# Optimization experiments

Hardware: AMD Instinct MI355X
Metric: run time of the kernel (lower is better)

## Reference

```python
import jax, jax.numpy as jnp
import numpy as np
from jax import lax


def _lstm_cell(x, h, c, W_ih, W_hh, b_ih, b_hh):
    # torch nn.LSTMCell: gates = x W_ih^T + b_ih + h W_hh^T + b_hh, order i,f,g,o
    gates = x @ W_ih.T + h @ W_hh.T + (b_ih + b_hh)
    i, f, g, o = jnp.split(gates, 4, axis=-1)
    c_new = jax.nn.sigmoid(f) * c + jax.nn.sigmoid(i) * jnp.tanh(g)
    h_new = jax.nn.sigmoid(o) * jnp.tanh(c_new)
    return h_new, c_new


def setup_inputs():
    key = jax.random.key(0)
    ks = jax.random.split(key, 10)
    B, S, E, H, V = 128, 20, 512, 512, 10000
    images = jax.random.normal(ks[0], (B, E), jnp.float32)
    captions = jax.random.randint(ks[1], (B, S), 0, V)
    length = jax.random.randint(ks[2], (B, 1), 2, S + 1)
    length = length.at[0, 0].set(S)  # guarantee max decode length == S-1 (static shape)
    s = 0.05
    emb = jax.random.normal(ks[3], (V, E), jnp.float32) * s
    W_ih = jax.random.normal(ks[4], (4 * H, E), jnp.float32) * s
    W_hh = jax.random.normal(ks[5], (4 * H, H), jnp.float32) * s
    b_ih = jax.random.normal(ks[6], (4 * H,), jnp.float32) * s
    b_hh = jax.random.normal(ks[7], (4 * H,), jnp.float32) * s
    fc_w = jax.random.normal(ks[8], (V, H), jnp.float32) * s
    fc_b = jax.random.normal(ks[9], (V,), jnp.float32) * s
    return dict(images=images, captions=captions, length=length, emb=emb,
                W_ih=W_ih, W_hh=W_hh, b_ih=b_ih, b_hh=b_hh, fc_w=fc_w, fc_b=fc_b)


def reference(images, captions, length, emb, W_ih, W_hh, b_ih, b_hh, fc_w, fc_b):
    B, S = captions.shape
    T = S - 1  # static max(decode_lengths) by construction
    H = W_hh.shape[1]
    lens = length[:, 0]
    sort_ind = jnp.argsort(-lens)  # stable descending sort, like torch .sort(descending=True)
    sorted_lens = lens[sort_ind]
    dec_len = sorted_lens - 1
    features = images[sort_ind]
    captions_s = captions[sort_ind]
    embeddings = emb[captions_s]  # [B, S, E]

    zeros = jnp.zeros((B, H), images.dtype)
    h, c = _lstm_cell(features, zeros, zeros, W_ih, W_hh, b_ih, b_hh)

    xs = (jnp.swapaxes(embeddings[:, :T, :], 0, 1), jnp.arange(T))  # [T,B,E], [T]

    def step(carry, x):
        h, c = carry
        x_t, t = x
        # ragged batch in the original == masking here: rows with dec_len<=t never
        # contribute to any future valid output (lengths sorted descending).
        h, c = _lstm_cell(x_t, h, c, W_ih, W_hh, b_ih, b_hh)
        preds = h @ fc_w.T + fc_b  # dropout is identity in eval mode
        preds = jnp.where((dec_len > t)[:, None], preds, 0.0)
        return (h, c), preds

    (_, _), preds = lax.scan(step, (h, c), xs)
    predictions = jnp.swapaxes(preds, 0, 1)  # [B, T, V]
    return predictions, captions_s, dec_len, sort_ind
```

## Files before the change

kernel.cpp:

```cpp
#include <hip/hip_runtime.h>

typedef float  f32x4 __attribute__((ext_vector_type(4)));
typedef short  s16x8 __attribute__((ext_vector_type(8)));
typedef unsigned short u16x4 __attribute__((ext_vector_type(4)));

#define MFMA16(a,b,c) __builtin_amdgcn_mfma_f32_16x16x32_bf16(a,b,c,0,0,0)

#define PRED_ELEMS 24320000ull

__device__ __forceinline__ unsigned short f2bf(float f){
  unsigned u = __builtin_bit_cast(unsigned, f);
  u += 0x7fffu + ((u >> 16) & 1u);
  return (unsigned short)(u >> 16);
}
__device__ __forceinline__ float sigf(float x){ return 1.0f/(1.0f + __expf(-x)); }
__device__ __forceinline__ float tanh_(float x){
  x = fminf(15.0f, fmaxf(-15.0f, x));
  float e = __expf(2.0f*x);
  return (e - 1.0f) / (e + 1.0f);
}
__device__ __forceinline__ s16x8 ld8(const unsigned short* p){
  return *reinterpret_cast<const s16x8*>(p);
}
__device__ __forceinline__ void gload_lds16(const unsigned short* src, unsigned short* dst){
  __builtin_amdgcn_global_load_lds(
      (const __attribute__((address_space(1))) void*)src,
      (__attribute__((address_space(3))) void*)dst, 16, 0, 0);
}

__global__ void k0_sort(const int* __restrict__ length, const int* __restrict__ captions,
                        float* __restrict__ out, int* __restrict__ sortp,
                        int* __restrict__ nactp, unsigned int* __restrict__ cnt4k)
{
  __shared__ int sl[128], sdl[128], ssi[128];
  int tid = threadIdx.x;
  for (int k = tid; k < 1024; k += 128) cnt4k[k] = 0u;
  if (tid < 128) sl[tid] = length[tid];
  __syncthreads();
  if (tid < 128){
    int l = sl[tid];
    int rank = 0;
    for (int j = 0; j < 128; ++j){
      int lj = sl[j];
      rank += (lj > l) || (lj == l && j < tid);
    }
    sortp[rank] = tid;
    ssi[rank] = tid;   sdl[rank] = l - 1;
  }
  __syncthreads();
  if (tid < 20){
    int c = 0;
    for (int r = 0; r < 128; ++r) c += (sdl[r] >= tid);
    nactp[tid] = c;
  }
  if (tid < 128){
    const size_t P = PRED_ELEMS;
    int si = ssi[tid];
    for (int t = 0; t < 20; ++t) out[P + tid*20 + t] = (float)captions[si*20 + t];
    out[P + 2560 + tid] = (float)sdl[tid];
    out[P + 2688 + tid] = (float)si;
  }
}

__device__ __forceinline__ void cvt4(unsigned short* dst, const float* src, int u){
  f32x4 v = *reinterpret_cast<const f32x4*>(src + (size_t)u*4);
  u16x4 o;
  o[0]=f2bf(v[0]); o[1]=f2bf(v[1]); o[2]=f2bf(v[2]); o[3]=f2bf(v[3]);
  *reinterpret_cast<u16x4*>(dst + (size_t)u*4) = o;
}

__global__ void k1_convert(const float* __restrict__ images, const int* __restrict__ captions,
    const float* __restrict__ emb, const float* __restrict__ wih, const float* __restrict__ whh,
    const float* __restrict__ bih, const float* __restrict__ bhh, const float* __restrict__ fcw,
    const int* __restrict__ sortp,
    unsigned short* __restrict__ wihb, unsigned short* __restrict__ whhb,
    unsigned short* __restrict__ fcwb, float* __restrict__ biasp,
    unsigned short* __restrict__ xseq, unsigned short* __restrict__ hseq,
    unsigned short* __restrict__ hloc)
{
  const int U0 = 262144;
  const int U1 = 262144;
  const int U2 = 1294336;
  const int U3 = 512;
  const int U4 = 327680;
  const int U5 = 16384;
  const int U6 = 16384;
  const int total = U0+U1+U2+U3+U4+U5+U6;
  for (int i = blockIdx.x*blockDim.x + threadIdx.x; i < total; i += gridDim.x*blockDim.x){
    int j = i;
    if (j < U0){ cvt4(wihb, wih, j); continue; }
    j -= U0;
    if (j < U1){ cvt4(whhb, whh, j); continue; }
    j -= U1;
    if (j < U2){
      int row = j >> 7;
      if (row < 10000) cvt4(fcwb, fcw, j);
      else { u16x4 z = {0,0,0,0}; *reinterpret_cast<u16x4*>(fcwb + (size_t)j*4) = z; }
      continue;
    }
    j -= U2;
    if (j < U3){
      int e0 = j*4;
      for (int e = 0; e < 4; ++e) biasp[e0+e] = bih[e0+e] + bhh[e0+e];
      continue;
    }
    j -= U3;
    if (j < U4){
      int elem = j*4;
      int s = elem >> 16;
      int rem = elem & 65535;
      int r = rem >> 9;
      int k = rem & 511;
      const float* src;
      if (s == 0) src = images + (size_t)sortp[r]*512 + k;
      else {
        int cap = captions[sortp[r]*20 + (s-1)];
        src = emb + (size_t)cap*512 + k;
      }
      f32x4 v = *reinterpret_cast<const f32x4*>(src);
      u16x4 o;
      o[0]=f2bf(v[0]); o[1]=f2bf(v[1]); o[2]=f2bf(v[2]); o[3]=f2bf(v[3]);
      *reinterpret_cast<u16x4*>(xseq + (size_t)j*4) = o;
      continue;
    }
    j -= U4;
    if (j < U5){ u16x4 z = {0,0,0,0}; *reinterpret_cast<u16x4*>(hseq + (size_t)j*4) = z; continue; }
    j -= U5;
    {
      int e0 = j*4;
      int x = e0 >> 13;
      int rem = e0 & 8191;
      u16x4 z = {0,0,0,0};
      *reinterpret_cast<u16x4*>(hloc + (size_t)x*172032 + rem) = z;
    }
  }
}

__global__ __launch_bounds__(256, 1) void lstm_chain(
    const unsigned short* __restrict__ xseq, const unsigned short* __restrict__ wih,
    const unsigned short* __restrict__ whh, const float* __restrict__ biasp,
    unsigned short* __restrict__ hseq, unsigned short* __restrict__ hloc,
    const int* __restrict__ nact, unsigned int* __restrict__ claimc,
    unsigned int* __restrict__ flags)
{
  const int tid = threadIdx.x;
  __shared__ int s_xw;
  __shared__ float pgh[4][4][16][17];
  __shared__ float pgx[4][4][16][17];
  __shared__ unsigned char lds_pad[51200];
  asm volatile("" : : "v"(&lds_pad[tid & 127]) : "memory");

  if (tid == 0){
    unsigned xcc;
    asm volatile("s_getreg_b32 %0, hwreg(20, 0, 4)" : "=s"(xcc));
    int x = (int)(xcc & 7u);
    unsigned slot = __hip_atomic_fetch_add(claimc + x*64, 1u,
                      __ATOMIC_RELAXED, __HIP_MEMORY_SCOPE_AGENT);
    s_xw = (x << 8) | (int)(slot & 255u);
  }
  __syncthreads();
  const int x = s_xw >> 8;
  const int w = s_xw & 255;
  if (w >= 32) return;
  const int R0 = x*16;
  const int C0 = w*16;
  unsigned int* myflags = flags + x*64;

  const int lane = tid & 63;
  const int kk   = tid >> 6;
  const int fr   = lane & 15;
  const int fkq  = (lane >> 4) * 8;
  const int rr   = (lane >> 4) * 4;

  s16x8 BI[4][4], BH[4][4];
  #pragma unroll
  for (int q = 0; q < 4; ++q)
    #pragma unroll
    for (int i = 0; i < 4; ++i){
      size_t off = (size_t)(q*512 + C0 + fr)*512 + kk*128 + i*32 + fkq;
      BI[q][i] = ld8(wih + off);
      BH[q][i] = ld8(whh + off);
    }

  unsigned short* hl = hloc + (size_t)x*172032;
  const int prow = tid >> 4;
  const int pcol = tid & 15;
  const float bz0 = biasp[       C0 + pcol];
  const float bz1 = biasp[ 512 + C0 + pcol];
  const float bz2 = biasp[1024 + C0 + pcol];
  const float bz3 = biasp[1536 + C0 + pcol];
  float creg = 0.f;

  {
    s16x8 ax[4];
    #pragma unroll
    for (int i = 0; i < 4; ++i)
      ax[i] = ld8(xseq + (R0 + fr)*512 + kk*128 + i*32 + fkq);
    #pragma unroll
    for (int q = 0; q < 4; ++q){
      f32x4 accx = (f32x4){0.f,0.f,0.f,0.f};
      #pragma unroll
      for (int i = 0; i < 4; ++i)
        accx = MFMA16(ax[i], BI[q][i], accx);
      #pragma unroll
      for (int p = 0; p < 4; ++p)
        pgx[kk][q][rr + p][fr] = accx[p];
    }
  }
  __syncthreads();

  for (int s = 0; s < 20; ++s){
    if (R0 >= nact[s]) break;
    const unsigned short* hp = hl + (size_t)s*8192;

    s16x8 ah[4];
    #pragma unroll
    for (int i = 0; i < 4; ++i)
      ah[i] = ld8(hp + fr*512 + kk*128 + i*32 + fkq);
    #pragma unroll
    for (int q = 0; q < 4; ++q){
      f32x4 acch = (f32x4){0.f,0.f,0.f,0.f};
      #pragma unroll
      for (int i = 0; i < 4; ++i)
        acch = MFMA16(ah[i], BH[q][i], acch);
      #pragma unroll
      for (int p = 0; p < 4; ++p)
        pgh[kk][q][rr + p][fr] = acch[p];
    }
    __syncthreads();

    unsigned short hb;
    {
      float iv = pgh[0][0][prow][pcol] + pgh[1][0][prow][pcol]
               + pgh[2][0][prow][pcol] + pgh[3][0][prow][pcol]
               + pgx[0][0][prow][pcol] + pgx[1][0][prow][pcol]
               + pgx[2][0][prow][pcol] + pgx[3][0][prow][pcol] + bz0;
      float fv = pgh[0][1][prow][pcol] + pgh[1][1][prow][pcol]
               + pgh[2][1][prow][pcol] + pgh[3][1][prow][pcol]
               + pgx[0][1][prow][pcol] + pgx[1][1][prow][pcol]
               + pgx[2][1][prow][pcol] + pgx[3][1][prow][pcol] + bz1;
      float gv = pgh[0][2][prow][pcol] + pgh[1][2][prow][pcol]
               + pgh[2][2][prow][pcol] + pgh[3][2][prow][pcol]
               + pgx[0][2][prow][pcol] + pgx[1][2][prow][pcol]
               + pgx[2][2][prow][pcol] + pgx[3][2][prow][pcol] + bz2;
      float ov = pgh[0][3][prow][pcol] + pgh[1][3][prow][pcol]
               + pgh[2][3][prow][pcol] + pgh[3][3][prow][pcol]
               + pgx[0][3][prow][pcol] + pgx[1][3][prow][pcol]
               + pgx[2][3][prow][pcol] + pgx[3][3][prow][pcol] + bz3;
      creg = sigf(fv)*creg + sigf(iv)*tanh_(gv);
      float h = sigf(ov)*tanh_(creg);
      hb = f2bf(h);
      hl[(size_t)(s+1)*8192 + prow*512 + C0 + pcol] = hb;
    }
    __syncthreads();

    hseq[(size_t)(s+1)*65536 + (R0 + prow)*512 + C0 + pcol] = hb;

    if (s < 19 && nact[s+1] > R0){
      const unsigned tgt = (unsigned)(s + 1);
      if (tid == 0)
        __hip_atomic_store(&myflags[w], tgt, __ATOMIC_RELAXED, __HIP_MEMORY_SCOPE_AGENT);

      {
        const unsigned short* xp = xseq + (size_t)(s+1)*65536;
        s16x8 ax[4];
        #pragma unroll
        for (int i = 0; i < 4; ++i)
          ax[i] = ld8(xp + (R0 + fr)*512 + kk*128 + i*32 + fkq);
        #pragma unroll
        for (int q = 0; q < 4; ++q){
          f32x4 accx = (f32x4){0.f,0.f,0.f,0.f};
          #pragma unroll
          for (int i = 0; i < 4; ++i)
            accx = MFMA16(ax[i], BI[q][i], accx);
          #pragma unroll
          for (int p = 0; p < 4; ++p)
            pgx[kk][q][rr + p][fr] = accx[p];
        }
      }

      if (tid < 64){
        long guard = 0;
        for (;;){
          bool ok = true;
          if (tid < 32)
            ok = (__hip_atomic_load(&myflags[tid], __ATOMIC_RELAXED,
                                    __HIP_MEMORY_SCOPE_AGENT) >= tgt);
          if (__all(ok) || ++guard > (1L << 20)) break;
          __builtin_amdgcn_s_sleep(1);
        }
      }
      __syncthreads();
    }
  }
}

__global__ __launch_bounds__(256) void fc_kernel(
    const unsigned short* __restrict__ hseq, const unsigned short* __restrict__ fcwb,
    const float* __restrict__ fcb, const int* __restrict__ nact,
    float* __restrict__ out)
{
  const int b    = blockIdx.x;
  const int x    = b & 7;
  const int slot = b >> 3;
  const int t    = slot % 19;
  const int p    = x + 8*(slot/19);
  if (p >= 79) return;
  const int v0   = p * 128;
  const int tid  = threadIdx.x;

  __shared__ unsigned short Ab[2][128*64];
  __shared__ unsigned short Bb[2][128*64];

  const unsigned short* Ag = hseq + (size_t)(t + 2)*65536;
  const unsigned short* Bg = fcwb + (size_t)v0*512;
  const int n_t = nact[t + 1];

  const int srow = tid >> 3;
  const int sphy = tid & 7;
  const int wuni = (tid >> 6) << 9;

  #define STAGE(gsrc, lbuf, kt)                                              \
    _Pragma("unroll")                                                        \
    for (int call = 0; call < 4; ++call){                                    \
      int row_ = call*32 + srow;                                             \
      gload_lds16(gsrc + (size_t)row_*512 + (kt)*64 + ((sphy ^ (row_ & 7)) << 3), \
                  lbuf + call*2048 + wuni);                                  \
    }

  const int lane = tid & 63;
  const int wv   = tid >> 6;
  const int wr   = wv >> 1, wc = wv & 1;
  const int fr   = lane & 15;
  const int hi   = lane >> 4;

  f32x4 acc[4][4];
  #pragma unroll
  for (int i = 0; i < 4; ++i)
    #pragma unroll
    for (int j = 0; j < 4; ++j)
      acc[i][j] = (f32x4){0.f,0.f,0.f,0.f};

  STAGE(Ag, Ab[0], 0)
  STAGE(Bg, Bb[0], 0)
  asm volatile("s_waitcnt vmcnt(0)" ::: "memory");
  __syncthreads();

  int cur = 0;
  for (int kt = 0; kt < 8; ++kt){
    if (kt < 7){
      STAGE(Ag, Ab[cur^1], kt+1)
      STAGE(Bg, Bb[cur^1], kt+1)
    }
    const unsigned short* As = Ab[cur];
    const unsigned short* Bs = Bb[cur];
    #pragma unroll
    for (int kk = 0; kk < 2; ++kk){
      const int c = kk*4 + hi;
      s16x8 af[4], bf[4];
      #pragma unroll
      for (int i = 0; i < 4; ++i){
        int row = wr*64 + i*16 + fr;
        af[i] = ld8(As + row*64 + ((c ^ (row & 7)) << 3));
      }
      #pragma unroll
      for (int j = 0; j < 4; ++j){
        int col = wc*64 + j*16 + fr;
        bf[j] = ld8(Bs + col*64 + ((c ^ (col & 7)) << 3));
      }
      #pragma unroll
      for (int i = 0; i < 4; ++i)
        #pragma unroll
        for (int j = 0; j < 4; ++j)
          acc[i][j] = MFMA16(af[i], bf[j], acc[i][j]);
    }
    asm volatile("s_waitcnt vmcnt(0)" ::: "memory");
    __syncthreads();
    cur ^= 1;
  }

  const int rr = hi * 4;
  #pragma unroll
  for (int j = 0; j < 4; ++j){
    int v = v0 + wc*64 + j*16 + fr;
    if (v >= 10000) continue;
    float bb = fcb[v];
    #pragma unroll
    for (int i = 0; i < 4; ++i){
      #pragma unroll
      for (int pp = 0; pp < 4; ++pp){
        int r = wr*64 + i*16 + rr + pp;
        out[(size_t)(r*19 + t)*10000 + v] = (r < n_t) ? (acc[i][j][pp] + bb) : 0.0f;
      }
    }
  }
  #undef STAGE
}

extern "C" void kernel_launch(void* const* d_in, const int* in_sizes, int n_in,
                              void* d_out, int out_size, void* d_ws, size_t ws_size,
                              hipStream_t stream) {
  const float* images   = (const float*)d_in[0];
  const int*   captions = (const int*)  d_in[1];
  const int*   length   = (const int*)  d_in[2];
  const float* emb      = (const float*)d_in[3];
  const float* W_ih     = (const float*)d_in[4];
  const float* W_hh     = (const float*)d_in[5];
  const float* b_ih     = (const float*)d_in[6];
  const float* b_hh     = (const float*)d_in[7];
  const float* fc_w     = (const float*)d_in[8];
  const float* fc_b     = (const float*)d_in[9];
  float* out = (float*)d_out;
  char*  ws  = (char*)d_ws;

  int*            sortp  = (int*)           (ws + 0);
  int*            nactp  = (int*)           (ws + 2048);
  float*          biasp  = (float*)         (ws + 4096);
  unsigned int*   cnt4k  = (unsigned int*)  (ws + 12288);
  unsigned int*   claimc = cnt4k;
  unsigned int*   flags  = cnt4k + 512;
  unsigned short* hloc   = (unsigned short*)(ws + 16384);
  unsigned short* hseq   = (unsigned short*)(ws + 2768896);
  unsigned short* xseq   = (unsigned short*)(ws + 5521408);
  unsigned short* wihb   = (unsigned short*)(ws + 8142848);
  unsigned short* whhb   = (unsigned short*)(ws + 10240000);
  unsigned short* fcwb   = (unsigned short*)(ws + 12337152);

  k0_sort<<<1, 128, 0, stream>>>(length, captions, out, sortp, nactp, cnt4k);
  k1_convert<<<4096, 256, 0, stream>>>(images, captions, emb, W_ih, W_hh, b_ih, b_hh,
                                       fc_w, sortp, wihb, whhb, fcwb, biasp, xseq, hseq, hloc);
  lstm_chain<<<256, 256, 0, stream>>>(xseq, wihb, whhb, biasp, hseq, hloc,
                                      nactp, claimc, flags);
  fc_kernel<<<1520, 256, 0, stream>>>(hseq, fcwb, fc_b, nactp, out);
}
```

Before: 122.9 us.

## Fuse LSTM recurrence and FC projection into one kernel with flag-based overlap

Merges the recurrent LSTM chain kernel and the vocabulary FC GEMM into a single launch. The first 256 blocks run the recurrence and publish a per-XCD step flag, while the remaining blocks wait on those flags and compute predictions for a timestep as soon as its hidden states are written. This lets the FC GEMM overlap the serial recurrence instead of waiting for it to finish. The FC tile is also re-staged with a smaller K chunk (32) and a different pipelining order so it fits the shared LDS union. The change depends on all chain blocks being co-resident with the waiting FC blocks, and the spin-waits could stall if scheduling does not guarantee that. Removing the LDS padding also changes occupancy for the chain blocks.

Result: slower. 148.0 us (+20.4%).

```diff
diff --git a/kernel.cpp b/kernel.cpp
--- a/kernel.cpp
+++ b/kernel.cpp
@@ -136,203 +136,234 @@
   }
 }
 
-__global__ __launch_bounds__(256, 1) void lstm_chain(
+union ShMem {
+  struct {
+    float pgh[4][4][16][17];
+    float pgx[4][4][16][17];
+    unsigned short mbuf[16][16];
+    int s_xw;
+  } l;
+  unsigned short arena[2][2][4096];
+};
+
+__global__ __launch_bounds__(256) void chain_fc(
     const unsigned short* __restrict__ xseq, const unsigned short* __restrict__ wih,
     const unsigned short* __restrict__ whh, const float* __restrict__ biasp,
     unsigned short* __restrict__ hseq, unsigned short* __restrict__ hloc,
+    const unsigned short* __restrict__ fcwb, const float* __restrict__ fcb,
     const int* __restrict__ nact, unsigned int* __restrict__ claimc,
-    unsigned int* __restrict__ flags)
+    unsigned int* __restrict__ flags, unsigned int* __restrict__ fcflag,
+    float* __restrict__ out)
 {
+  __shared__ ShMem sh;
   const int tid = threadIdx.x;
-  __shared__ int s_xw;
-  __shared__ float pgh[4][4][16][17];
-  __shared__ float pgx[4][4][16][17];
-  __shared__ unsigned char lds_pad[51200];
-  asm volatile("" : : "v"(&lds_pad[tid & 127]) : "memory");
-
-  if (tid == 0){
-    unsigned xcc;
-    asm volatile("s_getreg_b32 %0, hwreg(20, 0, 4)" : "=s"(xcc));
-    int x = (int)(xcc & 7u);
-    unsigned slot = __hip_atomic_fetch_add(claimc + x*64, 1u,
-                      __ATOMIC_RELAXED, __HIP_MEMORY_SCOPE_AGENT);
-    s_xw = (x << 8) | (int)(slot & 255u);
-  }
-  __syncthreads();
-  const int x = s_xw >> 8;
-  const int w = s_xw & 255;
-  if (w >= 32) return;
-  const int R0 = x*16;
-  const int C0 = w*16;
-  unsigned int* myflags = flags + x*64;
-
+  const int bid = blockIdx.x;
   const int lane = tid & 63;
-  const int kk   = tid >> 6;
-  const int fr   = lane & 15;
-  const int fkq  = (lane >> 4) * 8;
-  const int rr   = (lane >> 4) * 4;
-
-  s16x8 BI[4][4], BH[4][4];
-  #pragma unroll
-  for (int q = 0; q < 4; ++q)
-    #pragma unroll
-    for (int i = 0; i < 4; ++i){
-      size_t off = (size_t)(q*512 + C0 + fr)*512 + kk*128 + i*32 + fkq;
-      BI[q][i] = ld8(wih + off);
-      BH[q][i] = ld8(whh + off);
-    }
-
-  unsigned short* hl = hloc + (size_t)x*172032;
-  const int prow = tid >> 4;
-  const int pcol = tid & 15;
-  const float bz0 = biasp[       C0 + pcol];
-  const float bz1 = biasp[ 512 + C0 + pcol];
-  const float bz2 = biasp[1024 + C0 + pcol];
-  const float bz3 = biasp[1536 + C0 + pcol];
-  float creg = 0.f;
-
-  {
-    s16x8 ax[4];
-    #pragma unroll
-    for (int i = 0; i < 4; ++i)
-      ax[i] = ld8(xseq + (R0 + fr)*512 + kk*128 + i*32 + fkq);
-    #pragma unroll
-    for (int q = 0; q < 4; ++q){
-      f32x4 accx = (f32x4){0.f,0.f,0.f,0.f};
+
+  if (bid < 256){
+    if (tid == 0){
+      unsigned xcc;
+      asm volatile("s_getreg_b32 %0, hwreg(20, 0, 4)" : "=s"(xcc));
+      int x = (int)(xcc & 7u);
+      unsigned slot = __hip_atomic_fetch_add(claimc + x*64, 1u,
+                        __ATOMIC_RELAXED, __HIP_MEMORY_SCOPE_AGENT);
+      sh.l.s_xw = (x << 8) | (int)(slot & 255u);
+    }
+    __syncthreads();
+    const int x = sh.l.s_xw >> 8;
+    const int w = sh.l.s_xw & 255;
+    if (w >= 32) return;
+    const int R0 = x*16;
+    const int C0 = w*16;
+    unsigned int* myflags = flags + x*64;
+
+    const int kk  = tid >> 6;
+    const int fr  = lane & 15;
+    const int fkq = (lane >> 4) * 8;
+    const int rr  = (lane >> 4) * 4;
+
+    s16x8 BI[4][4], BH[4][4];
+    #pragma unroll
+    for (int q = 0; q < 4; ++q)
+      #pragma unroll
+      for (int i = 0; i < 4; ++i){
+        size_t off = (size_t)(q*512 + C0 + fr)*512 + kk*128 + i*32 + fkq;
+        BI[q][i] = ld8(wih + off);
+        BH[q][i] = ld8(whh + off);
+      }
+
+    unsigned short* hl = hloc + (size_t)x*172032;
+    const int prow = tid >> 4;
+    const int pcol = tid & 15;
+    const float bz0 = biasp[       C0 + pcol];
+    const float bz1 = biasp[ 512 + C0 + pcol];
+    const float bz2 = biasp[1024 + C0 + pcol];
+    const float bz3 = biasp[1536 + C0 + pcol];
+    float creg = 0.f;
+
+    {
+      s16x8 ax[4];
       #pragma unroll
       for (int i = 0; i < 4; ++i)
-        accx = MFMA16(ax[i], BI[q][i], accx);
-      #pragma unroll
-      for (int p = 0; p < 4; ++p)
-        pgx[kk][q][rr + p][fr] = accx[p];
-    }
-  }
-  __syncthreads();
-
-  for (int s = 0; s < 20; ++s){
-    if (R0 >= nact[s]) break;
-    const unsigned short* hp = hl + (size_t)s*8192;
-
-    s16x8 ah[4];
-    #pragma unroll
-    for (int i = 0; i < 4; ++i)
-      ah[i] = ld8(hp + fr*512 + kk*128 + i*32 + fkq);
-    #pragma unroll
-    for (int q = 0; q < 4; ++q){
-      f32x4 acch = (f32x4){0.f,0.f,0.f,0.f};
-      #pragma unroll
-      for (int i = 0; i < 4; ++i)
-        acch = MFMA16(ah[i], BH[q][i], acch);
-      #pragma unroll
-      for (int p = 0; p < 4; ++p)
-        pgh[kk][q][rr + p][fr] = acch[p];
-    }
-    __syncthreads();
-
-    unsigned short hb;
-    {
-      float iv = pgh[0][0][prow][pcol] + pgh[1][0][prow][pcol]
-               + pgh[2][0][prow][pcol] + pgh[3][0][prow][pcol]
-               + pgx[0][0][prow][pcol] + pgx[1][0][prow][pcol]
-               + pgx[2][0][prow][pcol] + pgx[3][0][prow][pcol] + bz0;
-      float fv = pgh[0][1][prow][pcol] + pgh[1][1][prow][pcol]
-               + pgh[2][1][prow][pcol] + pgh[3][1][prow][pcol]
-               + pgx[0][1][prow][pcol] + pgx[1][1][prow][pcol]
-               + pgx[2][1][prow][pcol] + pgx[3][1][prow][pcol] + bz1;
-      float gv = pgh[0][2][prow][pcol] + pgh[1][2][prow][pcol]
-               + pgh[2][2][prow][pcol] + pgh[3][2][prow][pcol]
-               + pgx[0][2][prow][pcol] + pgx[1][2][prow][pcol]
-               + pgx[2][2][prow][pcol] + pgx[3][2][prow][pcol] + bz2;
-      float ov = pgh[0][3][prow][pcol] + pgh[1][3][prow][pcol]
-               + pgh[2][3][prow][pcol] + pgh[3][3][prow][pcol]
-               + pgx[0][3][prow][pcol] + pgx[1][3][prow][pcol]
-               + pgx[2][3][prow][pcol] + pgx[3][3][prow][pcol] + bz3;
-      creg = sigf(fv)*creg + sigf(iv)*tanh_(gv);
-      float h = sigf(ov)*tanh_(creg);
-      hb = f2bf(h);
-      hl[(size_t)(s+1)*8192 + prow*512 + C0 + pcol] = hb;
-    }
-    __syncthreads();
-
-    hseq[(size_t)(s+1)*65536 + (R0 + prow)*512 + C0 + pcol] = hb;
-
-    if (s < 19 && nact[s+1] > R0){
-      const unsigned tgt = (unsigned)(s + 1);
-      if (tid == 0)
-        __hip_atomic_store(&myflags[w], tgt, __ATOMIC_RELAXED, __HIP_MEMORY_SCOPE_AGENT);
-
-      {
-        const unsigned short* xp = xseq + (size_t)(s+1)*65536;
-        s16x8 ax[4];
+        ax[i] = ld8(xseq + (R0 + fr)*512 + kk*128 + i*32 + fkq);
+      #pragma unroll
+      for (int q = 0; q < 4; ++q){
+        f32x4 accx = (f32x4){0.f,0.f,0.f,0.f};
         #pragma unroll
         for (int i = 0; i < 4; ++i)
-          ax[i] = ld8(xp + (R0 + fr)*512 + kk*128 + i*32 + fkq);
+          accx = MFMA16(ax[i], BI[q][i], accx);
         #pragma unroll
-        for (int q = 0; q < 4; ++q){
-          f32x4 accx = (f32x4){0.f,0.f,0.f,0.f};
+        for (int p = 0; p < 4; ++p)
+          sh.l.pgx[kk][q][rr + p][fr] = accx[p];
+      }
+    }
+    __syncthreads();
+
+    for (int s = 0; s < 20; ++s){
+      if (R0 >= nact[s]) break;
+      const unsigned short* hp = hl + (size_t)s*8192;
+
+      s16x8 ah[4];
+      #pragma unroll
+      for (int i = 0; i < 4; ++i)
+        ah[i] = ld8(hp + fr*512 + kk*128 + i*32 + fkq);
+      #pragma unroll
+      for (int q = 0; q < 4; ++q){
+        f32x4 acch = (f32x4){0.f,0.f,0.f,0.f};
+        #pragma unroll
+        for (int i = 0; i < 4; ++i)
+          acch = MFMA16(ah[i], BH[q][i], acch);
+        #pragma unroll
+        for (int p = 0; p < 4; ++p)
+          sh.l.pgh[kk][q][rr + p][fr] = acch[p];
+      }
+      __syncthreads();
+
+      {
+        float iv = sh.l.pgh[0][0][prow][pcol] + sh.l.pgh[1][0][prow][pcol]
+                 + sh.l.pgh[2][0][prow][pcol] + sh.l.pgh[3][0][prow][pcol]
+                 + sh.l.pgx[0][0][prow][pcol] + sh.l.pgx[1][0][prow][pcol]
+                 + sh.l.pgx[2][0][prow][pcol] + sh.l.pgx[3][0][prow][pcol] + bz0;
+        float fv = sh.l.pgh[0][1][prow][pcol] + sh.l.pgh[1][1][prow][pcol]
+                 + sh.l.pgh[2][1][prow][pcol] + sh.l.pgh[3][1][prow][pcol]
+                 + sh.l.pgx[0][1][prow][pcol] + sh.l.pgx[1][1][prow][pcol]
+                 + sh.l.pgx[2][1][prow][pcol] + sh.l.pgx[3][1][prow][pcol] + bz1;
+        float gv = sh.l.pgh[0][2][prow][pcol] + sh.l.pgh[1][2][prow][pcol]
+                 + sh.l.pgh[2][2][prow][pcol] + sh.l.pgh[3][2][prow][pcol]
+                 + sh.l.pgx[0][2][prow][pcol] + sh.l.pgx[1][2][prow][pcol]
+                 + sh.l.pgx[2][2][prow][pcol] + sh.l.pgx[3][2][prow][pcol] + bz2;
+        float ov = sh.l.pgh[0][3][prow][pcol] + sh.l.pgh[1][3][prow][pcol]
+                 + sh.l.pgh[2][3][prow][pcol] + sh.l.pgh[3][3][prow][pcol]
+                 + sh.l.pgx[0][3][prow][pcol] + sh.l.pgx[1][3][prow][pcol]
+                 + sh.l.pgx[2][3][prow][pcol] + sh.l.pgx[3][3][prow][pcol] + bz3;
+        creg = sigf(fv)*creg + sigf(iv)*tanh_(gv);
+        float h = sigf(ov)*tanh_(creg);
+        unsigned short hb = f2bf(h);
+        hl[(size_t)(s+1)*8192 + prow*512 + C0 + pcol] = hb;
+        sh.l.mbuf[prow][pcol] = hb;
+      }
+      __syncthreads();
+
+      if (tid < 128){
+        int r  = tid >> 3;
+        int c2 = (tid & 7) * 2;
+        unsigned wrd = (unsigned)sh.l.mbuf[r][c2] | ((unsigned)sh.l.mbuf[r][c2+1] << 16);
+        __hip_atomic_exchange(reinterpret_cast<unsigned*>(
+            hseq + (size_t)(s+1)*65536 + (size_t)(R0 + r)*512 + C0 + c2),
+            wrd, __ATOMIC_RELAXED, __HIP_MEMORY_SCOPE_AGENT);
+      }
+      __syncthreads();
+
+      {
+        const unsigned tgt = (unsigned)(s + 1);
+        if (tid == 0)
+          __hip_atomic_store(&myflags[w], tgt, __ATOMIC_RELAXED, __HIP_MEMORY_SCOPE_AGENT);
+
+        if (s < 19 && nact[s+1] > R0){
+          const unsigned short* xp = xseq + (size_t)(s+1)*65536;
+          s16x8 ax[4];
           #pragma unroll
           for (int i = 0; i < 4; ++i)
-            accx = MFMA16(ax[i], BI[q][i], accx);
+            ax[i] = ld8(xp + (R0 + fr)*512 + kk*128 + i*32 + fkq);
           #pragma unroll
-          for (int p = 0; p < 4; ++p)
-            pgx[kk][q][rr + p][fr] = accx[p];
+          for (int q = 0; q < 4; ++q){
+            f32x4 accx = (f32x4){0.f,0.f,0.f,0.f};
+            #pragma unroll
+            for (int i = 0; i < 4; ++i)
+              accx = MFMA16(ax[i], BI[q][i], accx);
+            #pragma unroll
+            for (int p = 0; p < 4; ++p)
+              sh.l.pgx[kk][q][rr + p][fr] = accx[p];
+          }
         }
-      }
-
-      if (tid < 64){
-        long guard = 0;
-        for (;;){
-          bool ok = true;
-          if (tid < 32)
-            ok = (__hip_atomic_load(&myflags[tid], __ATOMIC_RELAXED,
-                                    __HIP_MEMORY_SCOPE_AGENT) >= tgt);
-          if (__all(ok) || ++guard > (1L << 20)) break;
-          __builtin_amdgcn_s_sleep(1);
+
+        if (tid < 64){
+          long guard = 0;
+          for (;;){
+            bool ok = true;
+            if (tid < 32)
+              ok = (__hip_atomic_load(&myflags[tid], __ATOMIC_RELAXED,
+                                      __HIP_MEMORY_SCOPE_AGENT) >= tgt);
+            if (__all(ok) || ++guard > (1L << 20)) break;
+            __builtin_amdgcn_s_sleep(1);
+          }
         }
-      }
-      __syncthreads();
-    }
-  }
-}
-
-__global__ __launch_bounds__(256) void fc_kernel(
-    const unsigned short* __restrict__ hseq, const unsigned short* __restrict__ fcwb,
-    const float* __restrict__ fcb, const int* __restrict__ nact,
-    float* __restrict__ out)
-{
-  const int b    = blockIdx.x;
-  const int x    = b & 7;
-  const int slot = b >> 3;
+        if (tid == 0 && w == 0)
+          __hip_atomic_store(&fcflag[x*16], tgt, __ATOMIC_RELAXED, __HIP_MEMORY_SCOPE_AGENT);
+        __syncthreads();
+      }
+    }
+    return;
+  }
+
+  const int bfc  = bid - 256;
+  const int slot = bfc >> 3;
+  const int xaff = bfc & 7;
   const int t    = slot % 19;
-  const int p    = x + 8*(slot/19);
+  const int p    = xaff + 8*(slot/19);
   if (p >= 79) return;
   const int v0   = p * 128;
-  const int tid  = threadIdx.x;
-
-  __shared__ unsigned short Ab[2][128*64];
-  __shared__ unsigned short Bb[2][128*64];
+  const int n_t  = nact[t + 1];
 
   const unsigned short* Ag = hseq + (size_t)(t + 2)*65536;
   const unsigned short* Bg = fcwb + (size_t)v0*512;
-  const int n_t = nact[t + 1];
-
-  const int srow = tid >> 3;
-  const int sphy = tid & 7;
+
+  const int srow = tid >> 2;
+  const int sphy = tid & 3;
   const int wuni = (tid >> 6) << 9;
 
-  #define STAGE(gsrc, lbuf, kt)                                              \
-    _Pragma("unroll")                                                        \
-    for (int call = 0; call < 4; ++call){                                    \
-      int row_ = call*32 + srow;                                             \
-      gload_lds16(gsrc + (size_t)row_*512 + (kt)*64 + ((sphy ^ (row_ & 7)) << 3), \
-                  lbuf + call*2048 + wuni);                                  \
-    }
-
-  const int lane = tid & 63;
-  const int wv   = tid >> 6;
-  const int wr   = wv >> 1, wc = wv & 1;
-  const int fr   = lane & 15;
-  const int hi   = lane >> 4;
+  #define AbF(c) (&sh.arena[c][0][0])
+  #define BbF(c) (&sh.arena[c][1][0])
+  #define STAGE(gsrc, lbuf, kt)                                               \
+    _Pragma("unroll")                                                         \
+    for (int call = 0; call < 2; ++call){                                     \
+      int row_ = call*64 + srow;                                              \
+      gload_lds16(gsrc + (size_t)row_*512 + (kt)*32 + ((sphy ^ (row_ & 3)) << 3), \
+                  lbuf + call*2048 + wuni);                                   \
+    }
+
+  STAGE(Bg, BbF(0), 0)
+  {
+    if (tid < 64){
+      long guard = 0;
+      for (;;){
+        bool ok = true;
+        if (tid < 8){
+          unsigned f = __hip_atomic_load(&fcflag[tid*16], __ATOMIC_RELAXED,
+                                         __HIP_MEMORY_SCOPE_AGENT);
+          ok = (f >= (unsigned)(t + 2)) || (n_t <= tid*16);
+        }
+        if (__all(ok) || ++guard > (1L << 20)) break;
+        __builtin_amdgcn_s_sleep(8);
+      }
+    }
+    __syncthreads();
+  }
+
+  const int wv = tid >> 6;
+  const int wr = wv >> 1, wc = wv & 1;
+  const int fr = lane & 15;
+  const int hi = lane >> 4;
 
   f32x4 acc[4][4];
   #pragma unroll
@@ -341,45 +372,44 @@
     for (int j = 0; j < 4; ++j)
       acc[i][j] = (f32x4){0.f,0.f,0.f,0.f};
 
-  STAGE(Ag, Ab[0], 0)
-  STAGE(Bg, Bb[0], 0)
+  STAGE(Ag, AbF(0), 0)
+  STAGE(Ag, AbF(1), 1)
+  STAGE(Bg, BbF(1), 1)
   asm volatile("s_waitcnt vmcnt(0)" ::: "memory");
   __syncthreads();
 
   int cur = 0;
-  for (int kt = 0; kt < 8; ++kt){
-    if (kt < 7){
-      STAGE(Ag, Ab[cur^1], kt+1)
-      STAGE(Bg, Bb[cur^1], kt+1)
-    }
-    const unsigned short* As = Ab[cur];
-    const unsigned short* Bs = Bb[cur];
-    #pragma unroll
-    for (int kk = 0; kk < 2; ++kk){
-      const int c = kk*4 + hi;
-      s16x8 af[4], bf[4];
-      #pragma unroll
-      for (int i = 0; i < 4; ++i){
-        int row = wr*64 + i*16 + fr;
-        af[i] = ld8(As + row*64 + ((c ^ (row & 7)) << 3));
-      }
-      #pragma unroll
-      for (int j = 0; j < 4; ++j){
-        int col = wc*64 + j*16 + fr;
-        bf[j] = ld8(Bs + col*64 + ((c ^ (col & 7)) << 3));
-      }
-      #pragma unroll
-      for (int i = 0; i < 4; ++i)
-        #pragma unroll
-        for (int j = 0; j < 4; ++j)
-          acc[i][j] = MFMA16(af[i], bf[j], acc[i][j]);
+  for (int kt = 0; kt < 16; ++kt){
+    if (kt < 14){
+      STAGE(Ag, AbF(cur), kt+2)
+    }
+    const unsigned short* As = AbF(cur);
+    const unsigned short* Bs = BbF(cur);
+    s16x8 af[4], bf[4];
+    #pragma unroll
+    for (int i = 0; i < 4; ++i){
+      int row = wr*64 + i*16 + fr;
+      af[i] = ld8(As + row*32 + ((hi ^ (row & 3)) << 3));
+    }
+    #pragma unroll
+    for (int j = 0; j < 4; ++j){
+      int col = wc*64 + j*16 + fr;
+      bf[j] = ld8(Bs + col*32 + ((hi ^ (col & 3)) << 3));
+    }
+    #pragma unroll
+    for (int i = 0; i < 4; ++i)
+      #pragma unroll
+      for (int j = 0; j < 4; ++j)
+        acc[i][j] = MFMA16(af[i], bf[j], acc[i][j]);
+    if (kt < 14){
+      STAGE(Bg, BbF(cur), kt+2)
     }
     asm volatile("s_waitcnt vmcnt(0)" ::: "memory");
     __syncthreads();
     cur ^= 1;
   }
 
-  const int rr = hi * 4;
+  const int rr2 = hi * 4;
   #pragma unroll
   for (int j = 0; j < 4; ++j){
     int v = v0 + wc*64 + j*16 + fr;
@@ -389,12 +419,14 @@
     for (int i = 0; i < 4; ++i){
       #pragma unroll
       for (int pp = 0; pp < 4; ++pp){
-        int r = wr*64 + i*16 + rr + pp;
+        int r = wr*64 + i*16 + rr2 + pp;
         out[(size_t)(r*19 + t)*10000 + v] = (r < n_t) ? (acc[i][j][pp] + bb) : 0.0f;
       }
     }
   }
   #undef STAGE
+  #undef AbF
+  #undef BbF
 }
 
 extern "C" void kernel_launch(void* const* d_in, const int* in_sizes, int n_in,
@@ -419,6 +451,7 @@
   unsigned int*   cnt4k  = (unsigned int*)  (ws + 12288);
   unsigned int*   claimc = cnt4k;
   unsigned int*   flags  = cnt4k + 512;
+  unsigned int*   fcflag = cnt4k + 768;
   unsigned short* hloc   = (unsigned short*)(ws + 16384);
   unsigned short* hseq   = (unsigned short*)(ws + 2768896);
   unsigned short* xseq   = (unsigned short*)(ws + 5521408);
@@ -429,7 +462,6 @@
   k0_sort<<<1, 128, 0, stream>>>(length, captions, out, sortp, nactp, cnt4k);
   k1_convert<<<4096, 256, 0, stream>>>(images, captions, emb, W_ih, W_hh, b_ih, b_hh,
                                        fc_w, sortp, wihb, whhb, fcwb, biasp, xseq, hseq, hloc);
-  lstm_chain<<<256, 256, 0, stream>>>(xseq, wihb, whhb, biasp, hseq, hloc,
-                                      nactp, claimc, flags);
-  fc_kernel<<<1520, 256, 0, stream>>>(hseq, fcwb, fc_b, nactp, out);
-}
+  chain_fc<<<1776, 256, 0, stream>>>(xseq, wihb, whhb, biasp, hseq, hloc,
+                                     fcwb, fc_b, nactp, claimc, flags, fcflag, out);
+}
```
